# Kernel tuning notes

Hardware: AMD Instinct MI355X
Metric: run time of the kernel (lower is better)

The kernel has to match this reference:

```python
import jax, jax.numpy as jnp
import numpy as np

D = 128            # actual_dim
DM = 2 * D         # d_model = 256
DI = 2 * DM        # support-encoder inner dim = 512
H = 2 * DM         # LSTMCell hidden = 512
NUM_SYMBOLS = 200000
KNN_K = 10
PROCESS_STEPS = 4
BQ, BS, NN = 4096, 128, 64


def setup_inputs() -> dict:
    key = jax.random.key(0)
    ks = jax.random.split(key, 20)
    ri = lambda k, shape, hi: jax.random.randint(k, shape, 0, hi)
    rn = lambda k, shape, s=0.05: jax.random.normal(k, shape, jnp.float32) * s
    emb = rn(ks[0], (NUM_SYMBOLS + 1, D), 0.1).at[NUM_SYMBOLS].set(0.0)  # padding row
    return {
        "query": ri(ks[1], (BQ, 2), NUM_SYMBOLS),
        "support": ri(ks[2], (BS, 2), NUM_SYMBOLS),
        "q_l_conn": ri(ks[3], (BQ, NN, 2), NUM_SYMBOLS),
        "q_l_deg": ri(ks[4], (BQ,), NN),
        "q_r_conn": ri(ks[5], (BQ, NN, 2), NUM_SYMBOLS),
        "q_r_deg": ri(ks[6], (BQ,), NN),
        "s_l_conn": ri(ks[7], (BS, NN, 2), NUM_SYMBOLS),
        "s_l_deg": ri(ks[8], (BS,), NN),
        "s_r_conn": ri(ks[9], (BS, NN, 2), NUM_SYMBOLS),
        "s_r_deg": ri(ks[10], (BS,), NN),
        "emb": emb,
        "gcn_W": rn(ks[11], (D, 2 * D)),
        "gcn_wb": jnp.zeros((D,), jnp.float32),
        "gcn_b": jnp.zeros((D,), jnp.float32),
        "se_w1": rn(ks[12], (DI, DM)),
        "se_b1": jnp.zeros((DI,), jnp.float32),
        "se_w2": rn(ks[13], (DM, DI)),
        "se_b2": jnp.zeros((DM,), jnp.float32),
        "ln_g": jnp.ones((DM,), jnp.float32),
        "ln_b": jnp.zeros((DM,), jnp.float32),
        "W_ih": rn(ks[14], (4 * H, DM)),
        "W_hh": rn(ks[15], (4 * H, H)),
        "b_ih": jnp.zeros((4 * H,), jnp.float32),
        "b_hh": jnp.zeros((4 * H,), jnp.float32),
    }


def _cos(a, b, eps=1e-8):
    num = jnp.sum(a * b, -1)
    den = jnp.maximum(jnp.linalg.norm(a, axis=-1), eps) * jnp.maximum(jnp.linalg.norm(b, axis=-1), eps)
    return num / den


def _neighbor_encoder(emb, gcn_W, gcn_wb, gcn_b, conn, ent_ids):
    rel = emb[conn[..., 0]]                     # [B,N,D]
    ent = emb[conn[..., 1]]                     # [B,N,D]
    center = emb[ent_ids][:, None, :]           # [B,1,D]
    sim = _cos(center, ent)                     # [B,N]
    _, idx = jax.lax.top_k(sim, KNN_K)          # [B,K]
    rel_k = jnp.take_along_axis(rel, idx[..., None], axis=1)
    ent_k = jnp.take_along_axis(ent, idx[..., None], axis=1)
    cat = jnp.concatenate([rel_k, ent_k], -1)   # [B,K,2D]
    h = jnp.einsum('bkf,df->bkd', cat, gcn_W) + gcn_wb + gcn_b
    return jnp.tanh(h.mean(axis=1))             # [B,D]


def _support_encoder(x, w1, b1, w2, b2, g, b):
    # residual FFN + LayerNorm (GMatching SupportEncoder), dropout off (eval)
    out = jax.nn.relu(x @ w1.T + b1) @ w2.T + b2
    y = out + x
    mu = y.mean(-1, keepdims=True)
    var = ((y - mu) ** 2).mean(-1, keepdims=True)
    return (y - mu) / jnp.sqrt(var + 1e-5) * g + b


def _query_encoder(support, query, W_ih, W_hh, b_ih, b_hh):
    # GMatching attentive LSTM process block. support: [1,DM], query: [B,DM]
    B = query.shape[0]
    h_r = jnp.zeros((B, H), query.dtype)
    c = jnp.zeros((B, H), query.dtype)
    h = query
    for _ in range(PROCESS_STEPS):
        gates = query @ W_ih.T + b_ih + h_r @ W_hh.T + b_hh
        i, f, g_, o = jnp.split(gates, 4, axis=-1)  # torch LSTMCell gate order
        c = jax.nn.sigmoid(f) * c + jax.nn.sigmoid(i) * jnp.tanh(g_)
        h_new = jax.nn.sigmoid(o) * jnp.tanh(c)     # [B,H]
        h = query + h_new[:, :DM]                   # [B,DM]
        attn = jax.nn.softmax(h @ support.T, axis=1)  # [B,1]
        r = attn @ support                          # [B,DM]
        h_r = jnp.concatenate([h, r], axis=1)       # [B,H]
    return h


def reference(query, support, q_l_conn, q_l_deg, q_r_conn, q_r_deg,
              s_l_conn, s_l_deg, s_r_conn, s_r_deg,
              emb, gcn_W, gcn_wb, gcn_b,
              se_w1, se_b1, se_w2, se_b2, ln_g, ln_b,
              W_ih, W_hh, b_ih, b_hh):
    ne = lambda conn, ids: _neighbor_encoder(emb, gcn_W, gcn_wb, gcn_b, conn, ids)
    q_nb = jnp.concatenate([ne(q_l_conn, query[:, 0]), ne(q_r_conn, query[:, 1])], -1)    # [BQ,DM]
    s_nb = jnp.concatenate([ne(s_l_conn, support[:, 0]), ne(s_r_conn, support[:, 1])], -1)  # [BS,DM]
    se = lambda x: _support_encoder(x, se_w1, se_b1, se_w2, se_b2, ln_g, ln_b)
    support_g = se(s_nb).mean(axis=0, keepdims=True)  # [1,DM]
    query_g = se(q_nb)                                # [BQ,DM]
    qf = _query_encoder(support_g, query_g, W_ih, W_hh, b_ih, b_hh)
    l2 = lambda x: x / jnp.maximum(jnp.linalg.norm(x, axis=-1, keepdims=True), 1e-12)
    return (l2(qf) @ l2(support_g).T).squeeze(-1)     # [BQ]
```

## Files before the change

### kernel.cpp

```cpp
#include <hip/hip_runtime.h>
#include <hip/hip_bf16.h>

#define D   128
#define DM  256
#define DI  512
#define HH  512
#define KNN 10
#define NN  64
#define BQ  4096
#define BS  128
#define BM2 (BQ + BS)
#define G2  1024
#define GK  256
#define NSYM 200000

__device__ __forceinline__ float sigmoidf_(float x) {
    return 1.f / (1.f + __expf(-x));
}
__device__ __forceinline__ float tanh_fast(float x) {
    x = fminf(fmaxf(x, -20.f), 20.f);
    float e = __expf(2.f * x);
    return (e - 1.f) / (e + 1.f);
}
__device__ __forceinline__ ushort f2bf(float x) {
    union { float f; unsigned u; } v; v.f = x;
    unsigned r = (v.u + 0x7fffu + ((v.u >> 16) & 1u)) >> 16;
    return (ushort)r;
}

typedef __bf16  bf16x8  __attribute__((ext_vector_type(8)));
typedef float   floatx4 __attribute__((ext_vector_type(4)));

__global__ __launch_bounds__(256) void prep_kernel(
    const float* __restrict__ emb, float* __restrict__ norms,
    const float* __restrict__ W_ih, const float* __restrict__ W_hh,
    const float* __restrict__ b_ih, const float* __restrict__ b_hh,
    const float* __restrict__ se_w1, const float* __restrict__ se_w2,
    ushort* __restrict__ wih_bf, ushort* __restrict__ whh_bf,
    float* __restrict__ bsumP, ushort* __restrict__ w1_bf,
    ushort* __restrict__ w2_bf)
{
    int bid = blockIdx.x;
    int tid = threadIdx.x;
    if (bid < 50000) {
        int wave = tid >> 6, lane = tid & 63;
        int row = bid * 4 + wave;
        float2 v = *(const float2*)&emb[(size_t)row * D + lane * 2];
        float s = v.x * v.x + v.y * v.y;
        #pragma unroll
        for (int off = 32; off; off >>= 1) s += __shfl_xor(s, off);
        if (lane == 0) norms[row] = sqrtf(s);
    } else if (bid < 50000 + G2) {
        int n = bid - 50000;
        int bn = n >> 7, r = n & 127;
        int half = (r >> 6) & 1, j = (r >> 4) & 3, l = r & 15;
        int u = bn * 32 + half * 16 + l;
        int oldrow = j * 512 + u;
        wih_bf[n * 256 + tid] = f2bf(W_ih[(size_t)oldrow * DM + tid]);
        whh_bf[n * 256 + tid] = f2bf(W_hh[(size_t)oldrow * HH + tid]);
        if (tid == 0) bsumP[n] = b_ih[oldrow] + b_hh[oldrow];
    } else {
        int idx = (bid - 50000 - G2) * 256 + tid;
        w1_bf[idx] = f2bf(se_w1[idx]);
        w2_bf[idx] = f2bf(se_w2[idx]);
    }
}

__global__ __launch_bounds__(256) void ne_kernel(
    const int* __restrict__ q_l, const int* __restrict__ q_r,
    const int* __restrict__ q_ids,
    const int* __restrict__ s_l, const int* __restrict__ s_r,
    const int* __restrict__ s_ids,
    const float* __restrict__ emb, const float* __restrict__ norms,
    float* __restrict__ catm_out)
{
    int bid = blockIdx.x;
    const int *conn_l, *conn_r, *ids;
    int row;
    if (bid < BQ * 2) { conn_l = q_l; conn_r = q_r; ids = q_ids; row = bid >> 1; }
    else { conn_l = s_l; conn_r = s_r; ids = s_ids; row = (bid - BQ * 2) >> 1; }
    int side = bid & 1;
    const int* conn = (side ? conn_r : conn_l) + (size_t)row * NN * 2;
    int cid = ids[row * 2 + side];

    __shared__ int   connb[NN * 2];
    __shared__ float sim[NN];
    __shared__ int   selr[KNN], sele[KNN];

    int tid = threadIdx.x;
    int wave = tid >> 6, lane = tid & 63;
    int grp = lane >> 4, l16 = lane & 15;

    if (tid < NN * 2) connb[tid] = conn[tid];
    const float* cp = &emb[(size_t)cid * D + l16 * 8];
    float4 c4a = *(const float4*)cp;
    float4 c4b = *(const float4*)(cp + 4);
    float cnorm = fmaxf(norms[cid], 1e-8f);
    __syncthreads();

    float4 ea[4], eb[4];
    #pragma unroll
    for (int b = 0; b < 4; b++) {
        int j = wave * 16 + b * 4 + grp;
        int eid = connb[j * 2 + 1];
        const float* ep = &emb[(size_t)eid * D + l16 * 8];
        ea[b] = *(const float4*)ep;
        eb[b] = *(const float4*)(ep + 4);
    }
    #pragma unroll
    for (int b = 0; b < 4; b++) {
        int j = wave * 16 + b * 4 + grp;
        float dot = c4a.x * ea[b].x + c4a.y * ea[b].y + c4a.z * ea[b].z + c4a.w * ea[b].w
                  + c4b.x * eb[b].x + c4b.y * eb[b].y + c4b.z * eb[b].z + c4b.w * eb[b].w;
        #pragma unroll
        for (int off = 8; off; off >>= 1) dot += __shfl_xor(dot, off);
        if (l16 == 0) sim[j] = dot / cnorm;
    }
    __syncthreads();
    if (tid < NN) sim[tid] = sim[tid] / fmaxf(norms[connb[tid * 2 + 1]], 1e-8f);
    __syncthreads();

    if (wave == 0) {
        float s = sim[lane];
        int id = lane;
        for (int k = 0; k < KNN; k++) {
            float bs = s; int bi = id;
            #pragma unroll
            for (int off = 32; off; off >>= 1) {
                float os = __shfl_xor(bs, off);
                int   oi = __shfl_xor(bi, off);
                if (os > bs || (os == bs && oi < bi)) { bs = os; bi = oi; }
            }
            if (lane == 0) { selr[k] = connb[bi * 2]; sele[k] = connb[bi * 2 + 1]; }
            if (id == bi) s = -__builtin_inff();
        }
    }
    __syncthreads();

    float acc = 0.f;
    if (tid < D) {
        #pragma unroll
        for (int k = 0; k < KNN; k++) acc += emb[(size_t)selr[k] * D + tid];
    } else {
        int d = tid - D;
        #pragma unroll
        for (int k = 0; k < KNN; k++) acc += emb[(size_t)sele[k] * D + d];
    }
    catm_out[(size_t)bid * DM + tid] = acc * (1.f / KNN);
}

#define GR 16
__global__ __launch_bounds__(256) void gcn_kernel(
    const float* __restrict__ catm, const float* __restrict__ gcn_W,
    const float* __restrict__ gcn_wb, const float* __restrict__ gcn_b,
    float* __restrict__ out, ushort* __restrict__ out_bf)
{
    __shared__ float cs[GR][DM];
    __shared__ float pp[GR][DM];
    int tid = threadIdx.x;
    int m0 = blockIdx.x * GR;
    #pragma unroll
    for (int t = 0; t < 4; t++) {
        int chunk = tid + 256 * t;
        int r = chunk >> 6, c4 = chunk & 63;
        *(float4*)&cs[r][c4 * 4] = *(const float4*)&catm[(size_t)(m0 + r) * DM + c4 * 4];
    }
    __syncthreads();

    int d = tid & 127, half = tid >> 7;
    float a[GR];
    #pragma unroll
    for (int r = 0; r < GR; r++) a[r] = 0.f;
    const float4* W4 = (const float4*)(gcn_W + (size_t)d * DM + half * D);
    for (int f4 = 0; f4 < D / 4; ++f4) {
        float4 w = W4[f4];
        #pragma unroll
        for (int r = 0; r < GR; r++) {
            const float* c = &cs[r][half * D + f4 * 4];
            a[r] += w.x * c[0] + w.y * c[1] + w.z * c[2] + w.w * c[3];
        }
    }
    #pragma unroll
    for (int r = 0; r < GR; r++) pp[r][tid] = a[r];
    __syncthreads();
    if (tid < D) {
        #pragma unroll
        for (int r = 0; r < GR; r++) {
            float h = pp[r][tid] + pp[r][tid + D] + gcn_wb[tid] + gcn_b[tid];
            float th = tanh_fast(h);
            out[(size_t)(m0 + r) * D + tid] = th;
            out_bf[(size_t)(m0 + r) * D + tid] = f2bf(th);
        }
    }
}

#define BMT 128
#define BNT 128
#define BKT 64
#define LDP (BKT + 8)

#define GEMM_CORE(AP, BP, KDIM)                                               \
    floatx4 acc[4][4];                                                        \
    _Pragma("unroll")                                                         \
    for (int i = 0; i < 4; i++)                                               \
        _Pragma("unroll")                                                     \
        for (int j = 0; j < 4; j++) acc[i][j] = (floatx4){0.f, 0.f, 0.f, 0.f};\
    for (int k0 = 0; k0 < (KDIM); k0 += BKT) {                                \
        __syncthreads();                                                      \
        _Pragma("unroll")                                                     \
        for (int t = 0; t < 4; t++) {                                         \
            int chunk = tid + 256 * t;                                        \
            int r = chunk >> 3;                                               \
            int c8 = (chunk & 7) * 8;                                         \
            *(uint4*)&As[r][c8] = *(const uint4*)&(AP)[(size_t)(bm * BMT + r) * (KDIM) + k0 + c8]; \
            *(uint4*)&Bs[r][c8] = *(const uint4*)&(BP)[(size_t)(bn * BNT + r) * (KDIM) + k0 + c8]; \
        }                                                                     \
        __syncthreads();                                                      \
        _Pragma("unroll")                                                     \
        for (int kk = 0; kk < BKT; kk += 32) {                                \
            bf16x8 af[4], bf[4];                                              \
            _Pragma("unroll")                                                 \
            for (int i = 0; i < 4; i++)                                       \
                af[i] = *(const bf16x8*)&As[wm + i * 16 + l16][kk + quad * 8];\
            _Pragma("unroll")                                                 \
            for (int j = 0; j < 4; j++)                                       \
                bf[j] = *(const bf16x8*)&Bs[wn + j * 16 + l16][kk + quad * 8];\
            _Pragma("unroll")                                                 \
            for (int i = 0; i < 4; i++)                                       \
                _Pragma("unroll")                                             \
                for (int j = 0; j < 4; j++)                                   \
                    acc[i][j] = __builtin_amdgcn_mfma_f32_16x16x32_bf16(      \
                        af[i], bf[j], acc[i][j], 0, 0, 0);                    \
        }                                                                     \
    }

#define GEMM_PRE()                                                            \
    __shared__ __align__(16) ushort As[BMT][LDP];                             \
    __shared__ __align__(16) ushort Bs[BNT][LDP];                             \
    int tid = threadIdx.x;                                                    \
    int wave = tid >> 6, lane = tid & 63;                                     \
    int quad = lane >> 4, l16 = lane & 15;                                    \
    int bm = blockIdx.x, bn = blockIdx.y;                                     \
    int wm = (wave >> 1) * 64, wn = (wave & 1) * 64;                          \
    (void)wave;

__global__ __launch_bounds__(256) void se_gemm1_kernel(
    const ushort* __restrict__ A, const ushort* __restrict__ B,
    const float* __restrict__ b1, ushort* __restrict__ Cbf)
{
    GEMM_PRE();
    GEMM_CORE(A, B, DM);
    #pragma unroll
    for (int i = 0; i < 4; i++) {
        #pragma unroll
        for (int j = 0; j < 4; j++) {
            int row = bm * BMT + wm + i * 16 + quad * 4;
            int col = bn * BNT + wn + j * 16 + l16;
            float bb = b1[col];
            #pragma unroll
            for (int rr = 0; rr < 4; rr++)
                Cbf[(size_t)(row + rr) * DI + col] = f2bf(fmaxf(acc[i][j][rr] + bb, 0.f));
        }
    }
}

__global__ __launch_bounds__(256) void se_gemm2_kernel(
    const ushort* __restrict__ A, const ushort* __restrict__ B,
    const float* __restrict__ b2, const float* __restrict__ xres,
    float* __restrict__ C)
{
    GEMM_PRE();
    GEMM_CORE(A, B, DI);
    #pragma unroll
    for (int i = 0; i < 4; i++) {
        #pragma unroll
        for (int j = 0; j < 4; j++) {
            int row = bm * BMT + wm + i * 16 + quad * 4;
            int col = bn * BNT + wn + j * 16 + l16;
            float bb = b2[col];
            #pragma unroll
            for (int rr = 0; rr < 4; rr++)
                C[(size_t)(row + rr) * DM + col] =
                    acc[i][j][rr] + bb + xres[(size_t)(row + rr) * DM + col];
        }
    }
}

#define LN_ROWS 8
__global__ __launch_bounds__(256) void ln_kernel(
    const float* __restrict__ ys, const float* __restrict__ g,
    const float* __restrict__ b, float* __restrict__ outf,
    ushort* __restrict__ outbf)
{
    int tid = threadIdx.x;
    int wave = tid >> 6, lane = tid & 63;
    int r0 = blockIdx.x * LN_ROWS;
    for (int rr = 0; rr < 2; ++rr) {
        int r = r0 + wave * 2 + rr;
        float vals[4];
        float s = 0.f;
        #pragma unroll
        for (int e = 0; e < 4; e++) {
            vals[e] = ys[(size_t)r * DM + e * 64 + lane];
            s += vals[e];
        }
        #pragma unroll
        for (int off = 32; off; off >>= 1) s += __shfl_xor(s, off);
        float mu = s * (1.f / DM);
        float v = 0.f;
        #pragma unroll
        for (int e = 0; e < 4; e++) { float dd = vals[e] - mu; v += dd * dd; }
        #pragma unroll
        for (int off = 32; off; off >>= 1) v += __shfl_xor(v, off);
        float rstd = rsqrtf(v * (1.f / DM) + 1e-5f);
        #pragma unroll
        for (int e = 0; e < 4; e++) {
            int dd = e * 64 + lane;
            float ov = (vals[e] - mu) * rstd * g[dd] + b[dd];
            outf[(size_t)r * DM + dd] = ov;
            outbf[(size_t)r * DM + dd] = f2bf(ov);
        }
    }
}

__global__ __launch_bounds__(256) void sgw_kernel(
    const float* __restrict__ ln_f, const float* __restrict__ W_hh,
    const float* __restrict__ b_ih, const float* __restrict__ b_hh,
    float* __restrict__ sg, float* __restrict__ gaddP)
{
    __shared__ float s[DM];
    int tid = threadIdx.x;
    float a = 0.f;
    for (int r = 0; r < BS; r++) a += ln_f[(size_t)(BQ + r) * DM + tid];
    a *= (1.f / BS);
    s[tid] = a;
    if (blockIdx.x == 0) sg[tid] = a;
    __syncthreads();

    int idx = blockIdx.x * 256 + tid;
    int g = idx >> 8, u = idx & 255;
    int oldrow = g * 512 + u;
    const float4* w4 = (const float4*)(W_hh + (size_t)oldrow * HH + DM);
    float acc = 0.f;
    for (int f4 = 0; f4 < DM / 4; ++f4) {
        float4 w = w4[f4];
        acc += w.x * s[f4 * 4] + w.y * s[f4 * 4 + 1] + w.z * s[f4 * 4 + 2] + w.w * s[f4 * 4 + 3];
    }
    float bs = b_ih[oldrow] + b_hh[oldrow];
    int n = (u >> 5) * 128 + ((u >> 4) & 1) * 64 + g * 16 + (u & 15);
    gaddP[n] = bs + acc;
}

__global__ __launch_bounds__(256) void lstm_gemm0_kernel(
    const ushort* __restrict__ A, const ushort* __restrict__ B,
    const float* __restrict__ bsumP, const float* __restrict__ lnf,
    float* __restrict__ P0f, float* __restrict__ Cf, ushort* __restrict__ h_out)
{
    GEMM_PRE();
    GEMM_CORE(A, B, GK);
    int u = bn * 32 + (wn ? 16 : 0) + l16;
    size_t tile = (size_t)bm * 8 + bn;
    float b4[4];
    #pragma unroll
    for (int j = 0; j < 4; j++) b4[j] = bsumP[bn * 128 + wn + j * 16 + l16];
    #pragma unroll
    for (int i = 0; i < 4; i++) {
        int row = bm * BMT + wm + i * 16 + quad * 4;
        #pragma unroll
        for (int j = 0; j < 4; j++)
            *(floatx4*)&P0f[((tile * 16 + i * 4 + j) * 256 + tid) * 4] = acc[i][j];
        floatx4 cv4;
        #pragma unroll
        for (int rr = 0; rr < 4; rr++) {
            float iv = acc[i][0][rr] + b4[0];
            float gv = acc[i][2][rr] + b4[2];
            float ov = acc[i][3][rr] + b4[3];
            float cv = sigmoidf_(iv) * tanh_fast(gv);
            cv4[rr] = cv;
            float h = lnf[(size_t)(row + rr) * DM + u] + sigmoidf_(ov) * tanh_fast(cv);
            h_out[(size_t)(row + rr) * DM + u] = f2bf(h);
        }
        *(floatx4*)&Cf[((tile * 4 + i) * 256 + tid) * 4] = cv4;
    }
}

__global__ __launch_bounds__(256) void lstm_step_kernel(
    const ushort* __restrict__ A, const ushort* __restrict__ B,
    const float* __restrict__ P0f, const float* __restrict__ gaddP,
    const float* __restrict__ lnf, float* __restrict__ Cf,
    ushort* __restrict__ h_out, float* __restrict__ hf_out, int last)
{
    GEMM_PRE();
    GEMM_CORE(A, B, GK);
    int u = bn * 32 + (wn ? 16 : 0) + l16;
    size_t tile = (size_t)bm * 8 + bn;
    float g4[4];
    #pragma unroll
    for (int j = 0; j < 4; j++) g4[j] = gaddP[bn * 128 + wn + j * 16 + l16];
    #pragma unroll
    for (int i = 0; i < 4; i++) {
        int row = bm * BMT + wm + i * 16 + quad * 4;
        floatx4 p0[4];
        #pragma unroll
        for (int j = 0; j < 4; j++)
            p0[j] = *(const floatx4*)&P0f[((tile * 16 + i * 4 + j) * 256 + tid) * 4];
        floatx4 cprev = *(const floatx4*)&Cf[((tile * 4 + i) * 256 + tid) * 4];
        floatx4 cnew;
        #pragma unroll
        for (int rr = 0; rr < 4; rr++) {
            float iv = acc[i][0][rr] + p0[0][rr] + g4[0];
            float fv = acc[i][1][rr] + p0[1][rr] + g4[1];
            float gv = acc[i][2][rr] + p0[2][rr] + g4[2];
            float ov = acc[i][3][rr] + p0[3][rr] + g4[3];
            float cv = sigmoidf_(fv) * cprev[rr] + sigmoidf_(iv) * tanh_fast(gv);
            cnew[rr] = cv;
            float h = lnf[(size_t)(row + rr) * DM + u] + sigmoidf_(ov) * tanh_fast(cv);
            if (last) hf_out[(size_t)(row + rr) * DM + u] = h;
            else      h_out[(size_t)(row + rr) * DM + u] = f2bf(h);
        }
        *(floatx4*)&Cf[((tile * 4 + i) * 256 + tid) * 4] = cnew;
    }
}

__global__ __launch_bounds__(256) void final_kernel(
    const float* __restrict__ h_ws, const float* __restrict__ sg,
    float* __restrict__ outp)
{
    __shared__ float sgs[DM];
    int tid = threadIdx.x;
    sgs[tid] = sg[tid];
    __syncthreads();
    int wave = tid >> 6, lane = tid & 63;
    float sn = 0.f;
    #pragma unroll
    for (int e = 0; e < 4; e++) { float v = sgs[e * 64 + lane]; sn += v * v; }
    #pragma unroll
    for (int off = 32; off; off >>= 1) sn += __shfl_xor(sn, off);
    float sgnorm = fmaxf(sqrtf(sn), 1e-12f);

    int row = blockIdx.x * 4 + wave;
    const float* h = h_ws + (size_t)row * DM;
    float dot = 0.f, hn = 0.f;
    #pragma unroll
    for (int e = 0; e < 4; e++) {
        float hv = h[e * 64 + lane];
        dot += hv * sgs[e * 64 + lane];
        hn += hv * hv;
    }
    #pragma unroll
    for (int off = 32; off; off >>= 1) { dot += __shfl_xor(dot, off); hn += __shfl_xor(hn, off); }
    if (lane == 0) outp[row] = dot / (fmaxf(sqrtf(hn), 1e-12f) * sgnorm);
}

extern "C" void kernel_launch(void* const* d_in, const int* in_sizes, int n_in,
                              void* d_out, int out_size, void* d_ws, size_t ws_size,
                              hipStream_t stream)
{
    const int* query    = (const int*)d_in[0];
    const int* support  = (const int*)d_in[1];
    const int* q_l_conn = (const int*)d_in[2];
    const int* q_r_conn = (const int*)d_in[4];
    const int* s_l_conn = (const int*)d_in[6];
    const int* s_r_conn = (const int*)d_in[8];
    const float* emb    = (const float*)d_in[10];
    const float* gcn_W  = (const float*)d_in[11];
    const float* gcn_wb = (const float*)d_in[12];
    const float* gcn_b  = (const float*)d_in[13];
    const float* se_w1  = (const float*)d_in[14];
    const float* se_b1  = (const float*)d_in[15];
    const float* se_w2  = (const float*)d_in[16];
    const float* se_b2  = (const float*)d_in[17];
    const float* ln_g   = (const float*)d_in[18];
    const float* ln_b   = (const float*)d_in[19];
    const float* W_ih   = (const float*)d_in[20];
    const float* W_hh   = (const float*)d_in[21];
    const float* b_ih   = (const float*)d_in[22];
    const float* b_hh   = (const float*)d_in[23];
    float* out = (float*)d_out;

    char* wsb = (char*)d_ws;
    float*  xf     = (float*)wsb;  wsb += (size_t)BM2 * DM * 4;
    ushort* xb     = (ushort*)wsb; wsb += (size_t)BM2 * DM * 2;
    ushort* t1_bf  = (ushort*)wsb; wsb += (size_t)BM2 * DI * 2;
    float*  ys     = (float*)wsb;  wsb += (size_t)BM2 * DM * 4;
    float*  ln_f   = (float*)wsb;  wsb += (size_t)BM2 * DM * 4;
    ushort* ln_bf  = (ushort*)wsb; wsb += (size_t)BM2 * DM * 2;
    float*  sg     = (float*)wsb;  wsb += DM * 4;
    float*  bsumP  = (float*)wsb;  wsb += G2 * 4;
    float*  gaddP  = (float*)wsb;  wsb += G2 * 4;
    ushort* wih_bf = (ushort*)wsb; wsb += (size_t)G2 * DM * 2;
    ushort* whh_bf = (ushort*)wsb; wsb += (size_t)G2 * DM * 2;
    ushort* w1_bf  = (ushort*)wsb; wsb += (size_t)DI * DM * 2;
    ushort* w2_bf  = (ushort*)wsb; wsb += (size_t)DM * DI * 2;
    float*  norms  = (float*)wsb;  wsb += (size_t)NSYM * 4;
    float*  P0f    = (float*)wsb;  wsb += (size_t)BQ * G2 * 4;
    float*  Cf     = (float*)wsb;  wsb += (size_t)BQ * DM * 4;
    ushort* h_bfA  = (ushort*)wsb; wsb += (size_t)BQ * DM * 2;
    ushort* h_bfB  = (ushort*)wsb; wsb += (size_t)BQ * DM * 2;
    float*  h_f    = (float*)wsb;  wsb += (size_t)BQ * DM * 4;

    float* catm = P0f;

    prep_kernel<<<50000 + G2 + 512, 256, 0, stream>>>(
        emb, norms, W_ih, W_hh, b_ih, b_hh, se_w1, se_w2,
        wih_bf, whh_bf, bsumP, w1_bf, w2_bf);
    ne_kernel<<<BQ * 2 + BS * 2, 256, 0, stream>>>(
        q_l_conn, q_r_conn, query, s_l_conn, s_r_conn, support,
        emb, norms, catm);
    gcn_kernel<<<(BM2 * 2) / GR, 256, 0, stream>>>(catm, gcn_W, gcn_wb, gcn_b,
                                                   xf, xb);
    { dim3 g1(BM2 / BMT, DI / BNT);
      se_gemm1_kernel<<<g1, 256, 0, stream>>>(xb, w1_bf, se_b1, t1_bf); }
    { dim3 g2(BM2 / BMT, DM / BNT);
      se_gemm2_kernel<<<g2, 256, 0, stream>>>(t1_bf, w2_bf, se_b2, xf, ys); }
    ln_kernel<<<BM2 / LN_ROWS, 256, 0, stream>>>(ys, ln_g, ln_b, ln_f, ln_bf);
    sgw_kernel<<<G2 / 256, 256, 0, stream>>>(ln_f, W_hh, b_ih, b_hh, sg, gaddP);

    dim3 ggrid(BQ / BMT, G2 / BNT);
    lstm_gemm0_kernel<<<ggrid, 256, 0, stream>>>(ln_bf, wih_bf, bsumP, ln_f,
                                                 P0f, Cf, h_bfA);
    lstm_step_kernel<<<ggrid, 256, 0, stream>>>(h_bfA, whh_bf, P0f, gaddP, ln_f,
                                                Cf, h_bfB, h_f, 0);
    lstm_step_kernel<<<ggrid, 256, 0, stream>>>(h_bfB, whh_bf, P0f, gaddP, ln_f,
                                                Cf, h_bfA, h_f, 0);
    lstm_step_kernel<<<ggrid, 256, 0, stream>>>(h_bfA, whh_bf, P0f, gaddP, ln_f,
                                                Cf, h_bfB, h_f, 1);
    final_kernel<<<BQ / 4, 256, 0, stream>>>(h_f, sg, out);
}
```

Before: 407.2 us.

## Fuse post-gather stages into a persistent mega-kernel with grid barriers

Replaces the gcn, two support-encoder GEMMs, layernorm, support-gate, LSTM steps and final cosine kernels with one persistent kernel of 256 blocks. The stages are separated by a software grid-wide barrier built on atomics. LSTM state (P0 projections and cell state) now stays in registers across the steps instead of round-tripping through global memory. This removes many kernel launches and the P0/C traffic. In exchange, some stages run with few active blocks (e.g. 66 or 4), the spin barrier adds its own cost, and co-residency of all 256 blocks is assumed.

```diff
diff --git a/kernel.cpp b/kernel.cpp
--- a/kernel.cpp
+++ b/kernel.cpp
@@ -13,6 +13,7 @@
 #define G2  1024
 #define GK  256
 #define NSYM 200000
+#define NB  256
 
 __device__ __forceinline__ float sigmoidf_(float x) {
     return 1.f / (1.f + __expf(-x));
@@ -30,6 +31,24 @@
 
 typedef __bf16  bf16x8  __attribute__((ext_vector_type(8)));
 typedef float   floatx4 __attribute__((ext_vector_type(4)));
+
+__device__ __forceinline__ void gsync(unsigned* bar, unsigned* gen)
+{
+    __threadfence();
+    __syncthreads();
+    if (threadIdx.x == 0) {
+        unsigned g = __hip_atomic_load(gen, __ATOMIC_RELAXED, __HIP_MEMORY_SCOPE_AGENT);
+        unsigned old = __hip_atomic_fetch_add(bar, 1u, __ATOMIC_ACQ_REL, __HIP_MEMORY_SCOPE_AGENT);
+        if (old == NB - 1) {
+            __hip_atomic_store(bar, 0u, __ATOMIC_RELAXED, __HIP_MEMORY_SCOPE_AGENT);
+            __hip_atomic_store(gen, g + 1u, __ATOMIC_RELEASE, __HIP_MEMORY_SCOPE_AGENT);
+        } else {
+            while (__hip_atomic_load(gen, __ATOMIC_ACQUIRE, __HIP_MEMORY_SCOPE_AGENT) == g)
+                __builtin_amdgcn_s_sleep(8);
+        }
+    }
+    __syncthreads();
+}
 
 __global__ __launch_bounds__(256) void prep_kernel(
     const float* __restrict__ emb, float* __restrict__ norms,
@@ -38,7 +57,8 @@
     const float* __restrict__ se_w1, const float* __restrict__ se_w2,
     ushort* __restrict__ wih_bf, ushort* __restrict__ whh_bf,
     float* __restrict__ bsumP, ushort* __restrict__ w1_bf,
-    ushort* __restrict__ w2_bf)
+    ushort* __restrict__ w2_bf, unsigned* __restrict__ bar,
+    unsigned* __restrict__ gen)
 {
     int bid = blockIdx.x;
     int tid = threadIdx.x;
@@ -59,6 +79,7 @@
         wih_bf[n * 256 + tid] = f2bf(W_ih[(size_t)oldrow * DM + tid]);
         whh_bf[n * 256 + tid] = f2bf(W_hh[(size_t)oldrow * HH + tid]);
         if (tid == 0) bsumP[n] = b_ih[oldrow] + b_hh[oldrow];
+        if (n == 0 && tid == 1) { *bar = 0u; *gen = 0u; }
     } else {
         int idx = (bid - 50000 - G2) * 256 + tid;
         w1_bf[idx] = f2bf(se_w1[idx]);
@@ -149,307 +170,301 @@
     catm_out[(size_t)bid * DM + tid] = acc * (1.f / KNN);
 }
 
-#define GR 16
-__global__ __launch_bounds__(256) void gcn_kernel(
-    const float* __restrict__ catm, const float* __restrict__ gcn_W,
-    const float* __restrict__ gcn_wb, const float* __restrict__ gcn_b,
-    float* __restrict__ out, ushort* __restrict__ out_bf)
-{
-    __shared__ float cs[GR][DM];
-    __shared__ float pp[GR][DM];
-    int tid = threadIdx.x;
-    int m0 = blockIdx.x * GR;
-    #pragma unroll
-    for (int t = 0; t < 4; t++) {
-        int chunk = tid + 256 * t;
-        int r = chunk >> 6, c4 = chunk & 63;
-        *(float4*)&cs[r][c4 * 4] = *(const float4*)&catm[(size_t)(m0 + r) * DM + c4 * 4];
-    }
-    __syncthreads();
-
-    int d = tid & 127, half = tid >> 7;
-    float a[GR];
-    #pragma unroll
-    for (int r = 0; r < GR; r++) a[r] = 0.f;
-    const float4* W4 = (const float4*)(gcn_W + (size_t)d * DM + half * D);
-    for (int f4 = 0; f4 < D / 4; ++f4) {
-        float4 w = W4[f4];
-        #pragma unroll
-        for (int r = 0; r < GR; r++) {
-            const float* c = &cs[r][half * D + f4 * 4];
-            a[r] += w.x * c[0] + w.y * c[1] + w.z * c[2] + w.w * c[3];
-        }
-    }
-    #pragma unroll
-    for (int r = 0; r < GR; r++) pp[r][tid] = a[r];
-    __syncthreads();
-    if (tid < D) {
-        #pragma unroll
-        for (int r = 0; r < GR; r++) {
-            float h = pp[r][tid] + pp[r][tid + D] + gcn_wb[tid] + gcn_b[tid];
-            float th = tanh_fast(h);
-            out[(size_t)(m0 + r) * D + tid] = th;
-            out_bf[(size_t)(m0 + r) * D + tid] = f2bf(th);
-        }
-    }
-}
-
 #define BMT 128
 #define BNT 128
 #define BKT 64
 #define LDP (BKT + 8)
-
-#define GEMM_CORE(AP, BP, KDIM)                                               \
-    floatx4 acc[4][4];                                                        \
-    _Pragma("unroll")                                                         \
-    for (int i = 0; i < 4; i++)                                               \
-        _Pragma("unroll")                                                     \
-        for (int j = 0; j < 4; j++) acc[i][j] = (floatx4){0.f, 0.f, 0.f, 0.f};\
-    for (int k0 = 0; k0 < (KDIM); k0 += BKT) {                                \
-        __syncthreads();                                                      \
-        _Pragma("unroll")                                                     \
-        for (int t = 0; t < 4; t++) {                                         \
-            int chunk = tid + 256 * t;                                        \
-            int r = chunk >> 3;                                               \
-            int c8 = (chunk & 7) * 8;                                         \
-            *(uint4*)&As[r][c8] = *(const uint4*)&(AP)[(size_t)(bm * BMT + r) * (KDIM) + k0 + c8]; \
-            *(uint4*)&Bs[r][c8] = *(const uint4*)&(BP)[(size_t)(bn * BNT + r) * (KDIM) + k0 + c8]; \
-        }                                                                     \
-        __syncthreads();                                                      \
-        _Pragma("unroll")                                                     \
-        for (int kk = 0; kk < BKT; kk += 32) {                                \
-            bf16x8 af[4], bf[4];                                              \
-            _Pragma("unroll")                                                 \
-            for (int i = 0; i < 4; i++)                                       \
-                af[i] = *(const bf16x8*)&As[wm + i * 16 + l16][kk + quad * 8];\
-            _Pragma("unroll")                                                 \
-            for (int j = 0; j < 4; j++)                                       \
-                bf[j] = *(const bf16x8*)&Bs[wn + j * 16 + l16][kk + quad * 8];\
-            _Pragma("unroll")                                                 \
-            for (int i = 0; i < 4; i++)                                       \
-                _Pragma("unroll")                                             \
-                for (int j = 0; j < 4; j++)                                   \
-                    acc[i][j] = __builtin_amdgcn_mfma_f32_16x16x32_bf16(      \
-                        af[i], bf[j], acc[i][j], 0, 0, 0);                    \
-        }                                                                     \
-    }
-
-#define GEMM_PRE()                                                            \
-    __shared__ __align__(16) ushort As[BMT][LDP];                             \
-    __shared__ __align__(16) ushort Bs[BNT][LDP];                             \
-    int tid = threadIdx.x;                                                    \
-    int wave = tid >> 6, lane = tid & 63;                                     \
-    int quad = lane >> 4, l16 = lane & 15;                                    \
-    int bm = blockIdx.x, bn = blockIdx.y;                                     \
-    int wm = (wave >> 1) * 64, wn = (wave & 1) * 64;                          \
-    (void)wave;
-
-__global__ __launch_bounds__(256) void se_gemm1_kernel(
+#define GR  16
+
+template<int KDIM>
+__device__ __forceinline__ void gemm_core(
     const ushort* __restrict__ A, const ushort* __restrict__ B,
-    const float* __restrict__ b1, ushort* __restrict__ Cbf)
+    ushort (*As)[LDP], ushort (*Bs)[LDP], int tid,
+    int bm, int bn, int wm, int wn, int quad, int l16,
+    floatx4 (&acc)[4][4])
 {
-    GEMM_PRE();
-    GEMM_CORE(A, B, DM);
     #pragma unroll
-    for (int i = 0; i < 4; i++) {
+    for (int i = 0; i < 4; i++)
+        #pragma unroll
+        for (int j = 0; j < 4; j++) acc[i][j] = (floatx4){0.f, 0.f, 0.f, 0.f};
+    for (int k0 = 0; k0 < KDIM; k0 += BKT) {
+        __syncthreads();
+        #pragma unroll
+        for (int t = 0; t < 4; t++) {
+            int chunk = tid + 256 * t;
+            int r = chunk >> 3;
+            int c8 = (chunk & 7) * 8;
+            *(uint4*)&As[r][c8] = *(const uint4*)&A[(size_t)(bm * BMT + r) * KDIM + k0 + c8];
+            *(uint4*)&Bs[r][c8] = *(const uint4*)&B[(size_t)(bn * BNT + r) * KDIM + k0 + c8];
+        }
+        __syncthreads();
+        #pragma unroll
+        for (int kk = 0; kk < BKT; kk += 32) {
+            bf16x8 af[4], bf[4];
+            #pragma unroll
+            for (int i = 0; i < 4; i++)
+                af[i] = *(const bf16x8*)&As[wm + i * 16 + l16][kk + quad * 8];
+            #pragma unroll
+            for (int j = 0; j < 4; j++)
+                bf[j] = *(const bf16x8*)&Bs[wn + j * 16 + l16][kk + quad * 8];
+            #pragma unroll
+            for (int i = 0; i < 4; i++)
+                #pragma unroll
+                for (int j = 0; j < 4; j++)
+                    acc[i][j] = __builtin_amdgcn_mfma_f32_16x16x32_bf16(
+                        af[i], bf[j], acc[i][j], 0, 0, 0);
+        }
+    }
+}
+
+__global__ __launch_bounds__(256, 1) void mega_kernel(
+    const float* __restrict__ catm, const float* __restrict__ gcn_W,
+    const float* __restrict__ gcn_wb, const float* __restrict__ gcn_b,
+    float* __restrict__ xf, ushort* __restrict__ xb,
+    const ushort* __restrict__ w1_bf, const float* __restrict__ b1,
+    ushort* __restrict__ t1_bf,
+    const ushort* __restrict__ w2_bf, const float* __restrict__ b2,
+    float* __restrict__ ys,
+    const float* __restrict__ ln_g, const float* __restrict__ ln_b,
+    float* __restrict__ ln_f, ushort* __restrict__ ln_bf,
+    const float* __restrict__ W_hh, const float* __restrict__ b_ih,
+    const float* __restrict__ b_hh,
+    float* __restrict__ sg, float* __restrict__ gaddP,
+    const ushort* __restrict__ wih_bf, const ushort* __restrict__ whh_bf,
+    const float* __restrict__ bsumP,
+    ushort* __restrict__ h_bfA, ushort* __restrict__ h_bfB,
+    float* __restrict__ h_f, float* __restrict__ outp,
+    unsigned* __restrict__ bar, unsigned* __restrict__ gen)
+{
+    __shared__ __align__(16) char smem[2 * BMT * LDP * 2];
+    ushort (*As)[LDP] = (ushort(*)[LDP])smem;
+    ushort (*Bs)[LDP] = (ushort(*)[LDP])(smem + BMT * LDP * 2);
+
+    int tid = threadIdx.x;
+    int bid = blockIdx.x;
+    int wave = tid >> 6, lane = tid & 63;
+    int quad = lane >> 4, l16 = lane & 15;
+    int wm = (wave >> 1) * 64, wn = (wave & 1) * 64;
+
+    {
+        float (*cs)[DM] = (float(*)[DM])smem;
+        float (*pp)[DM] = (float(*)[DM])(smem + GR * DM * 4);
+        for (int t = bid; t < (BM2 * 2) / GR; t += NB) {
+            int m0 = t * GR;
+            #pragma unroll
+            for (int tt = 0; tt < 4; tt++) {
+                int chunk = tid + 256 * tt;
+                int r = chunk >> 6, c4 = chunk & 63;
+                *(float4*)&cs[r][c4 * 4] = *(const float4*)&catm[(size_t)(m0 + r) * DM + c4 * 4];
+            }
+            __syncthreads();
+            int d = tid & 127, half = tid >> 7;
+            float a[GR];
+            #pragma unroll
+            for (int r = 0; r < GR; r++) a[r] = 0.f;
+            const float4* W4 = (const float4*)(gcn_W + (size_t)d * DM + half * D);
+            for (int f4 = 0; f4 < D / 4; ++f4) {
+                float4 w = W4[f4];
+                #pragma unroll
+                for (int r = 0; r < GR; r++) {
+                    const float* c = &cs[r][half * D + f4 * 4];
+                    a[r] += w.x * c[0] + w.y * c[1] + w.z * c[2] + w.w * c[3];
+                }
+            }
+            #pragma unroll
+            for (int r = 0; r < GR; r++) pp[r][tid] = a[r];
+            __syncthreads();
+            if (tid < D) {
+                #pragma unroll
+                for (int r = 0; r < GR; r++) {
+                    float h = pp[r][tid] + pp[r][tid + D] + gcn_wb[tid] + gcn_b[tid];
+                    float th = tanh_fast(h);
+                    xf[(size_t)(m0 + r) * D + tid] = th;
+                    xb[(size_t)(m0 + r) * D + tid] = f2bf(th);
+                }
+            }
+            __syncthreads();
+        }
+    }
+    gsync(bar, gen);
+
+    if (bid < 132) {
+        int bm = bid % 33, bn = bid / 33;
+        floatx4 acc[4][4];
+        gemm_core<DM>(xb, w1_bf, As, Bs, tid, bm, bn, wm, wn, quad, l16, acc);
+        #pragma unroll
+        for (int i = 0; i < 4; i++)
+            #pragma unroll
+            for (int j = 0; j < 4; j++) {
+                int row = bm * BMT + wm + i * 16 + quad * 4;
+                int col = bn * BNT + wn + j * 16 + l16;
+                float bb = b1[col];
+                #pragma unroll
+                for (int rr = 0; rr < 4; rr++)
+                    t1_bf[(size_t)(row + rr) * DI + col] = f2bf(fmaxf(acc[i][j][rr] + bb, 0.f));
+            }
+    }
+    gsync(bar, gen);
+
+    if (bid < 66) {
+        int bm = bid % 33, bn = bid / 33;
+        floatx4 acc[4][4];
+        gemm_core<DI>(t1_bf, w2_bf, As, Bs, tid, bm, bn, wm, wn, quad, l16, acc);
+        #pragma unroll
+        for (int i = 0; i < 4; i++)
+            #pragma unroll
+            for (int j = 0; j < 4; j++) {
+                int row = bm * BMT + wm + i * 16 + quad * 4;
+                int col = bn * BNT + wn + j * 16 + l16;
+                float bb = b2[col];
+                #pragma unroll
+                for (int rr = 0; rr < 4; rr++)
+                    ys[(size_t)(row + rr) * DM + col] =
+                        acc[i][j][rr] + bb + xf[(size_t)(row + rr) * DM + col];
+            }
+    }
+    gsync(bar, gen);
+
+    for (int gidx = bid; gidx < BM2 / 8; gidx += NB) {
+        int r = gidx * 8 + wave * 2;
+        for (int rr = 0; rr < 2; ++rr, ++r) {
+            float vals[4];
+            float s = 0.f;
+            #pragma unroll
+            for (int e = 0; e < 4; e++) {
+                vals[e] = ys[(size_t)r * DM + e * 64 + lane];
+                s += vals[e];
+            }
+            #pragma unroll
+            for (int off = 32; off; off >>= 1) s += __shfl_xor(s, off);
+            float mu = s * (1.f / DM);
+            float v = 0.f;
+            #pragma unroll
+            for (int e = 0; e < 4; e++) { float dd = vals[e] - mu; v += dd * dd; }
+            #pragma unroll
+            for (int off = 32; off; off >>= 1) v += __shfl_xor(v, off);
+            float rstd = rsqrtf(v * (1.f / DM) + 1e-5f);
+            #pragma unroll
+            for (int e = 0; e < 4; e++) {
+                int dd = e * 64 + lane;
+                float ov = (vals[e] - mu) * rstd * ln_g[dd] + ln_b[dd];
+                ln_f[(size_t)r * DM + dd] = ov;
+                ln_bf[(size_t)r * DM + dd] = f2bf(ov);
+            }
+        }
+    }
+    gsync(bar, gen);
+
+    if (bid < 4) {
+        float* s = (float*)smem;
+        float a = 0.f;
+        for (int r = 0; r < BS; r++) a += ln_f[(size_t)(BQ + r) * DM + tid];
+        a *= (1.f / BS);
+        s[tid] = a;
+        if (bid == 0) sg[tid] = a;
+        __syncthreads();
+        int idx = bid * 256 + tid;
+        int g = idx >> 8, u = idx & 255;
+        int oldrow = g * 512 + u;
+        const float4* w4 = (const float4*)(W_hh + (size_t)oldrow * HH + DM);
+        float acc = 0.f;
+        for (int f4 = 0; f4 < DM / 4; ++f4) {
+            float4 w = w4[f4];
+            acc += w.x * s[f4 * 4] + w.y * s[f4 * 4 + 1] + w.z * s[f4 * 4 + 2] + w.w * s[f4 * 4 + 3];
+        }
+        float bs = b_ih[oldrow] + b_hh[oldrow];
+        int n = (u >> 5) * 128 + ((u >> 4) & 1) * 64 + g * 16 + (u & 15);
+        gaddP[n] = bs + acc;
+    }
+    gsync(bar, gen);
+
+    {
+        int bm = bid >> 3, bn = bid & 7;
+        int u = bn * 32 + (wn ? 16 : 0) + l16;
+
+        floatx4 P0[4][4];
+        floatx4 cfr[4];
+        float b4[4], g4[4];
         #pragma unroll
         for (int j = 0; j < 4; j++) {
-            int row = bm * BMT + wm + i * 16 + quad * 4;
-            int col = bn * BNT + wn + j * 16 + l16;
-            float bb = b1[col];
-            #pragma unroll
-            for (int rr = 0; rr < 4; rr++)
-                Cbf[(size_t)(row + rr) * DI + col] = f2bf(fmaxf(acc[i][j][rr] + bb, 0.f));
-        }
-    }
-}
-
-__global__ __launch_bounds__(256) void se_gemm2_kernel(
-    const ushort* __restrict__ A, const ushort* __restrict__ B,
-    const float* __restrict__ b2, const float* __restrict__ xres,
-    float* __restrict__ C)
-{
-    GEMM_PRE();
-    GEMM_CORE(A, B, DI);
-    #pragma unroll
-    for (int i = 0; i < 4; i++) {
-        #pragma unroll
-        for (int j = 0; j < 4; j++) {
-            int row = bm * BMT + wm + i * 16 + quad * 4;
-            int col = bn * BNT + wn + j * 16 + l16;
-            float bb = b2[col];
-            #pragma unroll
-            for (int rr = 0; rr < 4; rr++)
-                C[(size_t)(row + rr) * DM + col] =
-                    acc[i][j][rr] + bb + xres[(size_t)(row + rr) * DM + col];
-        }
-    }
-}
-
-#define LN_ROWS 8
-__global__ __launch_bounds__(256) void ln_kernel(
-    const float* __restrict__ ys, const float* __restrict__ g,
-    const float* __restrict__ b, float* __restrict__ outf,
-    ushort* __restrict__ outbf)
-{
-    int tid = threadIdx.x;
-    int wave = tid >> 6, lane = tid & 63;
-    int r0 = blockIdx.x * LN_ROWS;
-    for (int rr = 0; rr < 2; ++rr) {
-        int r = r0 + wave * 2 + rr;
-        float vals[4];
-        float s = 0.f;
-        #pragma unroll
-        for (int e = 0; e < 4; e++) {
-            vals[e] = ys[(size_t)r * DM + e * 64 + lane];
-            s += vals[e];
-        }
-        #pragma unroll
-        for (int off = 32; off; off >>= 1) s += __shfl_xor(s, off);
-        float mu = s * (1.f / DM);
-        float v = 0.f;
-        #pragma unroll
-        for (int e = 0; e < 4; e++) { float dd = vals[e] - mu; v += dd * dd; }
-        #pragma unroll
-        for (int off = 32; off; off >>= 1) v += __shfl_xor(v, off);
-        float rstd = rsqrtf(v * (1.f / DM) + 1e-5f);
-        #pragma unroll
-        for (int e = 0; e < 4; e++) {
-            int dd = e * 64 + lane;
-            float ov = (vals[e] - mu) * rstd * g[dd] + b[dd];
-            outf[(size_t)r * DM + dd] = ov;
-            outbf[(size_t)r * DM + dd] = f2bf(ov);
-        }
-    }
-}
-
-__global__ __launch_bounds__(256) void sgw_kernel(
-    const float* __restrict__ ln_f, const float* __restrict__ W_hh,
-    const float* __restrict__ b_ih, const float* __restrict__ b_hh,
-    float* __restrict__ sg, float* __restrict__ gaddP)
-{
-    __shared__ float s[DM];
-    int tid = threadIdx.x;
-    float a = 0.f;
-    for (int r = 0; r < BS; r++) a += ln_f[(size_t)(BQ + r) * DM + tid];
-    a *= (1.f / BS);
-    s[tid] = a;
-    if (blockIdx.x == 0) sg[tid] = a;
-    __syncthreads();
-
-    int idx = blockIdx.x * 256 + tid;
-    int g = idx >> 8, u = idx & 255;
-    int oldrow = g * 512 + u;
-    const float4* w4 = (const float4*)(W_hh + (size_t)oldrow * HH + DM);
-    float acc = 0.f;
-    for (int f4 = 0; f4 < DM / 4; ++f4) {
-        float4 w = w4[f4];
-        acc += w.x * s[f4 * 4] + w.y * s[f4 * 4 + 1] + w.z * s[f4 * 4 + 2] + w.w * s[f4 * 4 + 3];
-    }
-    float bs = b_ih[oldrow] + b_hh[oldrow];
-    int n = (u >> 5) * 128 + ((u >> 4) & 1) * 64 + g * 16 + (u & 15);
-    gaddP[n] = bs + acc;
-}
-
-__global__ __launch_bounds__(256) void lstm_gemm0_kernel(
-    const ushort* __restrict__ A, const ushort* __restrict__ B,
-    const float* __restrict__ bsumP, const float* __restrict__ lnf,
-    float* __restrict__ P0f, float* __restrict__ Cf, ushort* __restrict__ h_out)
-{
-    GEMM_PRE();
-    GEMM_CORE(A, B, GK);
-    int u = bn * 32 + (wn ? 16 : 0) + l16;
-    size_t tile = (size_t)bm * 8 + bn;
-    float b4[4];
-    #pragma unroll
-    for (int j = 0; j < 4; j++) b4[j] = bsumP[bn * 128 + wn + j * 16 + l16];
-    #pragma unroll
-    for (int i = 0; i < 4; i++) {
-        int row = bm * BMT + wm + i * 16 + quad * 4;
-        #pragma unroll
-        for (int j = 0; j < 4; j++)
-            *(floatx4*)&P0f[((tile * 16 + i * 4 + j) * 256 + tid) * 4] = acc[i][j];
-        floatx4 cv4;
-        #pragma unroll
-        for (int rr = 0; rr < 4; rr++) {
-            float iv = acc[i][0][rr] + b4[0];
-            float gv = acc[i][2][rr] + b4[2];
-            float ov = acc[i][3][rr] + b4[3];
-            float cv = sigmoidf_(iv) * tanh_fast(gv);
-            cv4[rr] = cv;
-            float h = lnf[(size_t)(row + rr) * DM + u] + sigmoidf_(ov) * tanh_fast(cv);
-            h_out[(size_t)(row + rr) * DM + u] = f2bf(h);
-        }
-        *(floatx4*)&Cf[((tile * 4 + i) * 256 + tid) * 4] = cv4;
-    }
-}
-
-__global__ __launch_bounds__(256) void lstm_step_kernel(
-    const ushort* __restrict__ A, const ushort* __restrict__ B,
-    const float* __restrict__ P0f, const float* __restrict__ gaddP,
-    const float* __restrict__ lnf, float* __restrict__ Cf,
-    ushort* __restrict__ h_out, float* __restrict__ hf_out, int last)
-{
-    GEMM_PRE();
-    GEMM_CORE(A, B, GK);
-    int u = bn * 32 + (wn ? 16 : 0) + l16;
-    size_t tile = (size_t)bm * 8 + bn;
-    float g4[4];
-    #pragma unroll
-    for (int j = 0; j < 4; j++) g4[j] = gaddP[bn * 128 + wn + j * 16 + l16];
-    #pragma unroll
-    for (int i = 0; i < 4; i++) {
-        int row = bm * BMT + wm + i * 16 + quad * 4;
-        floatx4 p0[4];
-        #pragma unroll
-        for (int j = 0; j < 4; j++)
-            p0[j] = *(const floatx4*)&P0f[((tile * 16 + i * 4 + j) * 256 + tid) * 4];
-        floatx4 cprev = *(const floatx4*)&Cf[((tile * 4 + i) * 256 + tid) * 4];
-        floatx4 cnew;
-        #pragma unroll
-        for (int rr = 0; rr < 4; rr++) {
-            float iv = acc[i][0][rr] + p0[0][rr] + g4[0];
-            float fv = acc[i][1][rr] + p0[1][rr] + g4[1];
-            float gv = acc[i][2][rr] + p0[2][rr] + g4[2];
-            float ov = acc[i][3][rr] + p0[3][rr] + g4[3];
-            float cv = sigmoidf_(fv) * cprev[rr] + sigmoidf_(iv) * tanh_fast(gv);
-            cnew[rr] = cv;
-            float h = lnf[(size_t)(row + rr) * DM + u] + sigmoidf_(ov) * tanh_fast(cv);
-            if (last) hf_out[(size_t)(row + rr) * DM + u] = h;
-            else      h_out[(size_t)(row + rr) * DM + u] = f2bf(h);
-        }
-        *(floatx4*)&Cf[((tile * 4 + i) * 256 + tid) * 4] = cnew;
-    }
-}
-
-__global__ __launch_bounds__(256) void final_kernel(
-    const float* __restrict__ h_ws, const float* __restrict__ sg,
-    float* __restrict__ outp)
-{
-    __shared__ float sgs[DM];
-    int tid = threadIdx.x;
-    sgs[tid] = sg[tid];
-    __syncthreads();
-    int wave = tid >> 6, lane = tid & 63;
-    float sn = 0.f;
-    #pragma unroll
-    for (int e = 0; e < 4; e++) { float v = sgs[e * 64 + lane]; sn += v * v; }
-    #pragma unroll
-    for (int off = 32; off; off >>= 1) sn += __shfl_xor(sn, off);
-    float sgnorm = fmaxf(sqrtf(sn), 1e-12f);
-
-    int row = blockIdx.x * 4 + wave;
-    const float* h = h_ws + (size_t)row * DM;
-    float dot = 0.f, hn = 0.f;
-    #pragma unroll
-    for (int e = 0; e < 4; e++) {
-        float hv = h[e * 64 + lane];
-        dot += hv * sgs[e * 64 + lane];
-        hn += hv * hv;
-    }
-    #pragma unroll
-    for (int off = 32; off; off >>= 1) { dot += __shfl_xor(dot, off); hn += __shfl_xor(hn, off); }
-    if (lane == 0) outp[row] = dot / (fmaxf(sqrtf(hn), 1e-12f) * sgnorm);
+            b4[j] = bsumP[bn * 128 + wn + j * 16 + l16];
+            g4[j] = gaddP[bn * 128 + wn + j * 16 + l16];
+        }
+
+        {
+            floatx4 acc[4][4];
+            gemm_core<GK>(ln_bf, wih_bf, As, Bs, tid, bm, bn, wm, wn, quad, l16, acc);
+            #pragma unroll
+            for (int i = 0; i < 4; i++) {
+                int row = bm * BMT + wm + i * 16 + quad * 4;
+                #pragma unroll
+                for (int j = 0; j < 4; j++) P0[i][j] = acc[i][j];
+                #pragma unroll
+                for (int rr = 0; rr < 4; rr++) {
+                    float iv = acc[i][0][rr] + b4[0];
+                    float gv = acc[i][2][rr] + b4[2];
+                    float ov = acc[i][3][rr] + b4[3];
+                    float cv = sigmoidf_(iv) * tanh_fast(gv);
+                    cfr[i][rr] = cv;
+                    float h = ln_f[(size_t)(row + rr) * DM + u] + sigmoidf_(ov) * tanh_fast(cv);
+                    h_bfA[(size_t)(row + rr) * DM + u] = f2bf(h);
+                }
+            }
+        }
+        gsync(bar, gen);
+
+        const ushort* hin = h_bfA;
+        ushort* hout = h_bfB;
+        for (int step = 0; step < 3; step++) {
+            int last = (step == 2);
+            floatx4 acc[4][4];
+            gemm_core<GK>(hin, whh_bf, As, Bs, tid, bm, bn, wm, wn, quad, l16, acc);
+            #pragma unroll
+            for (int i = 0; i < 4; i++) {
+                int row = bm * BMT + wm + i * 16 + quad * 4;
+                #pragma unroll
+                for (int rr = 0; rr < 4; rr++) {
+                    float iv = acc[i][0][rr] + P0[i][0][rr] + g4[0];
+                    float fv = acc[i][1][rr] + P0[i][1][rr] + g4[1];
+                    float gv = acc[i][2][rr] + P0[i][2][rr] + g4[2];
+                    float ov = acc[i][3][rr] + P0[i][3][rr] + g4[3];
+                    float cv = sigmoidf_(fv) * cfr[i][rr] + sigmoidf_(iv) * tanh_fast(gv);
+                    cfr[i][rr] = cv;
+                    float h = ln_f[(size_t)(row + rr) * DM + u] + sigmoidf_(ov) * tanh_fast(cv);
+                    if (last) h_f[(size_t)(row + rr) * DM + u] = h;
+                    else      hout[(size_t)(row + rr) * DM + u] = f2bf(h);
+                }
+            }
+            gsync(bar, gen);
+            const ushort* tmp = hin; hin = hout; hout = (ushort*)tmp;
+        }
+    }
+
+    {
+        float* sgs = (float*)smem;
+        sgs[tid] = sg[tid];
+        __syncthreads();
+        float sn = 0.f;
+        #pragma unroll
+        for (int e = 0; e < 4; e++) { float v = sgs[e * 64 + lane]; sn += v * v; }
+        #pragma unroll
+        for (int off = 32; off; off >>= 1) sn += __shfl_xor(sn, off);
+        float sgnorm = fmaxf(sqrtf(sn), 1e-12f);
+        for (int it = 0; it < 4; it++) {
+            int row = bid * 16 + it * 4 + wave;
+            const float* h = h_f + (size_t)row * DM;
+            float dot = 0.f, hn = 0.f;
+            #pragma unroll
+            for (int e = 0; e < 4; e++) {
+                float hv = h[e * 64 + lane];
+                dot += hv * sgs[e * 64 + lane];
+                hn += hv * hv;
+            }
+            #pragma unroll
+            for (int off = 32; off; off >>= 1) { dot += __shfl_xor(dot, off); hn += __shfl_xor(hn, off); }
+            if (lane == 0) outp[row] = dot / (fmaxf(sqrtf(hn), 1e-12f) * sgnorm);
+        }
+    }
 }
 
 extern "C" void kernel_launch(void* const* d_in, const int* in_sizes, int n_in,
@@ -479,6 +494,7 @@
     float* out = (float*)d_out;
 
     char* wsb = (char*)d_ws;
+    float*  catm   = (float*)wsb;  wsb += (size_t)(BM2 * 2) * DM * 4;
     float*  xf     = (float*)wsb;  wsb += (size_t)BM2 * DM * 4;
     ushort* xb     = (ushort*)wsb; wsb += (size_t)BM2 * DM * 2;
     ushort* t1_bf  = (ushort*)wsb; wsb += (size_t)BM2 * DI * 2;
@@ -493,37 +509,23 @@
     ushort* w1_bf  = (ushort*)wsb; wsb += (size_t)DI * DM * 2;
     ushort* w2_bf  = (ushort*)wsb; wsb += (size_t)DM * DI * 2;
     float*  norms  = (float*)wsb;  wsb += (size_t)NSYM * 4;
-    float*  P0f    = (float*)wsb;  wsb += (size_t)BQ * G2 * 4;
-    float*  Cf     = (float*)wsb;  wsb += (size_t)BQ * DM * 4;
     ushort* h_bfA  = (ushort*)wsb; wsb += (size_t)BQ * DM * 2;
     ushort* h_bfB  = (ushort*)wsb; wsb += (size_t)BQ * DM * 2;
     float*  h_f    = (float*)wsb;  wsb += (size_t)BQ * DM * 4;
-
-    float* catm = P0f;
+    unsigned* bar  = (unsigned*)wsb; wsb += 256;
+    unsigned* gen  = (unsigned*)(wsb); wsb += 256;
 
     prep_kernel<<<50000 + G2 + 512, 256, 0, stream>>>(
         emb, norms, W_ih, W_hh, b_ih, b_hh, se_w1, se_w2,
-        wih_bf, whh_bf, bsumP, w1_bf, w2_bf);
+        wih_bf, whh_bf, bsumP, w1_bf, w2_bf, bar, gen);
     ne_kernel<<<BQ * 2 + BS * 2, 256, 0, stream>>>(
         q_l_conn, q_r_conn, query, s_l_conn, s_r_conn, support,
         emb, norms, catm);
-    gcn_kernel<<<(BM2 * 2) / GR, 256, 0, stream>>>(catm, gcn_W, gcn_wb, gcn_b,
-                                                   xf, xb);
-    { dim3 g1(BM2 / BMT, DI / BNT);
-      se_gemm1_kernel<<<g1, 256, 0, stream>>>(xb, w1_bf, se_b1, t1_bf); }
-    { dim3 g2(BM2 / BMT, DM / BNT);
-      se_gemm2_kernel<<<g2, 256, 0, stream>>>(t1_bf, w2_bf, se_b2, xf, ys); }
-    ln_kernel<<<BM2 / LN_ROWS, 256, 0, stream>>>(ys, ln_g, ln_b, ln_f, ln_bf);
-    sgw_kernel<<<G2 / 256, 256, 0, stream>>>(ln_f, W_hh, b_ih, b_hh, sg, gaddP);
-
-    dim3 ggrid(BQ / BMT, G2 / BNT);
-    lstm_gemm0_kernel<<<ggrid, 256, 0, stream>>>(ln_bf, wih_bf, bsumP, ln_f,
-                                                 P0f, Cf, h_bfA);
-    lstm_step_kernel<<<ggrid, 256, 0, stream>>>(h_bfA, whh_bf, P0f, gaddP, ln_f,
-                                                Cf, h_bfB, h_f, 0);
-    lstm_step_kernel<<<ggrid, 256, 0, stream>>>(h_bfB, whh_bf, P0f, gaddP, ln_f,
-                                                Cf, h_bfA, h_f, 0);
-    lstm_step_kernel<<<ggrid, 256, 0, stream>>>(h_bfA, whh_bf, P0f, gaddP, ln_f,
-                                                Cf, h_bfB, h_f, 1);
-    final_kernel<<<BQ / 4, 256, 0, stream>>>(h_f, sg, out);
-}
+    mega_kernel<<<NB, 256, 0, stream>>>(
+        catm, gcn_W, gcn_wb, gcn_b, xf, xb,
+        w1_bf, se_b1, t1_bf, w2_bf, se_b2, ys,
+        ln_g, ln_b, ln_f, ln_bf,
+        W_hh, b_ih, b_hh, sg, gaddP,
+        wih_bf, whh_bf, bsumP,
+        h_bfA, h_bfB, h_f, out, bar, gen);
+}
```

New measurement: 810.4 us. +99.0%, slower.
